# Kernel tuning notes

Measured on AMD Instinct MI355X. Metric: run time of the kernel, lower is better.

Reference implementation:

```python
import jax, jax.numpy as jnp
import numpy as np

B, S, H, NH = 2, 2048, 1024, 16
HD = H // NH  # head_dim = 64
ROPE_BASE = 10000.0


def _rope(x):
    # x: [B, NH, S, HD]; LLaMA-style half-split rotary embedding
    s, d = x.shape[2], x.shape[3]
    inv_freq = 1.0 / (ROPE_BASE ** (jnp.arange(0, d, 2, dtype=jnp.float32) / d))  # [d/2]
    ang = jnp.arange(s, dtype=jnp.float32)[:, None] * inv_freq[None, :]            # [S, d/2]
    cos, sin = jnp.cos(ang), jnp.sin(ang)
    x1, x2 = x[..., : d // 2], x[..., d // 2:]
    return jnp.concatenate([x1 * cos - x2 * sin, x1 * sin + x2 * cos], axis=-1)


def setup_inputs() -> dict:
    key = jax.random.key(0)
    ks = jax.random.split(key, 9)
    hidden_states = jax.random.normal(ks[0], (B, S, H), dtype=jnp.float32)
    # causal mask: True = attend
    causal = jnp.tril(jnp.ones((S, S), dtype=bool))
    attention_mask = jnp.broadcast_to(causal[None, None, :, :], (B, 1, S, S))
    std = 0.02
    wq = jax.random.normal(ks[1], (H, NH * HD), dtype=jnp.float32) * std
    wk = jax.random.normal(ks[2], (H, NH * HD), dtype=jnp.float32) * std
    wv = jax.random.normal(ks[3], (H, NH * HD), dtype=jnp.float32) * std
    wo = jax.random.normal(ks[4], (NH * HD, H), dtype=jnp.float32) * std
    bq = jnp.zeros((NH * HD,), dtype=jnp.float32)
    bk = jnp.zeros((NH * HD,), dtype=jnp.float32)
    bv = jnp.zeros((NH * HD,), dtype=jnp.float32)
    bo = jnp.zeros((H,), dtype=jnp.float32)
    return {"hidden_states": hidden_states, "attention_mask": attention_mask,
            "wq": wq, "bq": bq, "wk": wk, "bk": bk, "wv": wv, "bv": bv,
            "wo": wo, "bo": bo}


def _split_heads(x):
    b, s, _ = x.shape
    return jnp.transpose(x.reshape(b, s, NH, HD), (0, 2, 1, 3))


def reference(hidden_states, attention_mask, wq, bq, wk, bk, wv, bv, wo, bo):
    q = _split_heads(hidden_states @ wq + bq)  # [B,NH,S,HD]
    k = _split_heads(hidden_states @ wk + bk)
    v = _split_heads(hidden_states @ wv + bv)
    q = _rope(q)
    k = _rope(k)
    scores = jnp.einsum('bhqd,bhkd->bhqk', q, k) / jnp.sqrt(jnp.float32(HD))
    scores = jnp.where(attention_mask, scores, jnp.float32(-1e9))
    weights = jax.nn.softmax(scores, axis=-1)
    attn = jnp.einsum('bhqk,bhkv->bhqv', weights, v)  # [B,NH,S,HD]
    attn = jnp.transpose(attn, (0, 2, 1, 3)).reshape(hidden_states.shape[0], attn.shape[2], H)
    return attn @ wo + bo
```

## Files before the change

### kernel.cpp

```cpp
#include <hip/hip_runtime.h>
#include <math.h>

typedef short bf16x8 __attribute__((ext_vector_type(8)));
typedef float f32x4  __attribute__((ext_vector_type(4)));

__device__ __forceinline__ unsigned short f2bf(float f) {
    union { float f; unsigned u; } v; v.f = f;
    unsigned r = v.u + 0x7FFFu + ((v.u >> 16) & 1u);
    return (unsigned short)(r >> 16);
}

#define GLDS16(gp, lp) __builtin_amdgcn_global_load_lds( \
    (const __attribute__((address_space(1))) void*)(gp), \
    (__attribute__((address_space(3))) void*)(lp), 16, 0, 0)


__global__ __launch_bounds__(256)
void prep(const float* __restrict__ X, unsigned short* __restrict__ Xb,
          const float* __restrict__ w0, const float* __restrict__ w1,
          const float* __restrict__ w2, const float* __restrict__ w3,
          unsigned short* o0, unsigned short* o1,
          unsigned short* o2, unsigned short* o3)
{
    const int z = blockIdx.z;
    if (z >= 4) {
        const int lb = (z - 4) * 256 + blockIdx.y * 16 + blockIdx.x;
        const size_t t = (size_t)lb * 256 + threadIdx.x;
        const float4 a = *(const float4*)(X + t * 8);
        const float4 b = *(const float4*)(X + t * 8 + 4);
        unsigned short u[8] = { f2bf(a.x), f2bf(a.y), f2bf(a.z), f2bf(a.w),
                                f2bf(b.x), f2bf(b.y), f2bf(b.z), f2bf(b.w) };
        *(int4*)(Xb + t * 8) = *(int4*)u;
        return;
    }
    const float* W; unsigned short* O;
    switch (z) {
        case 0: W = w0; O = o0; break;
        case 1: W = w1; O = o1; break;
        case 2: W = w2; O = o2; break;
        default: W = w3; O = o3; break;
    }
    __shared__ float T[64][65];
    const int tid = threadIdx.x;
    const int n0 = blockIdx.x * 64, k0 = blockIdx.y * 64;
    #pragma unroll
    for (int i = 0; i < 4; i++) {
        const int k = (tid >> 4) + i * 16, n4 = (tid & 15) * 4;
        const float4 v = *(const float4*)(W + (size_t)(k0 + k) * 1024 + n0 + n4);
        T[k][n4] = v.x; T[k][n4+1] = v.y; T[k][n4+2] = v.z; T[k][n4+3] = v.w;
    }
    __syncthreads();
    if (z == 3) {
        #pragma unroll
        for (int i = 0; i < 4; i++) {
            const int n = (tid >> 4) + i * 16, k4 = (tid & 15) * 4;
            unsigned short u[4];
            #pragma unroll
            for (int j = 0; j < 4; j++) {
                const int q = k4 + j;
                const int p = (q & 3) * 16 + (q >> 2);
                const int d = (p & 3) * 16 + (p >> 2);
                u[j] = f2bf(T[d][n]);
            }
            *(int2*)(O + (size_t)(n0 + n) * 1024 + k0 + k4) = *(int2*)u;
        }
    } else {
        #pragma unroll
        for (int i = 0; i < 4; i++) {
            const int n = (tid >> 4) + i * 16, k4 = (tid & 15) * 4;
            unsigned short u[4] = { f2bf(T[k4][n]), f2bf(T[k4+1][n]),
                                    f2bf(T[k4+2][n]), f2bf(T[k4+3][n]) };
            *(int2*)(O + (size_t)(n0 + n) * 1024 + k0 + k4) = *(int2*)u;
        }
    }
}

__global__ __launch_bounds__(256)
void qkv_gemm(const unsigned short* __restrict__ Xb,
              const unsigned short* __restrict__ Wtq, const unsigned short* __restrict__ Wtk,
              const unsigned short* __restrict__ Wtv,
              const float* __restrict__ bq, const float* __restrict__ bk,
              const float* __restrict__ bv,
              unsigned short* __restrict__ Qb, unsigned short* __restrict__ Kb,
              unsigned short* __restrict__ Vtb)
{
    const unsigned short* Wt; const float* bias; unsigned short* Out;
    const int z = blockIdx.z;
    if (z == 0)      { Wt = Wtq; bias = bq; Out = Qb; }
    else if (z == 1) { Wt = Wtk; bias = bk; Out = Kb; }
    else             { Wt = Wtv; bias = bv; Out = Vtb; }

    __shared__ unsigned short Sh[128 * 72];
    unsigned short* As = Sh;
    unsigned short* Bs = Sh + 128 * 32;
    unsigned short* T  = Sh;

    const int tid = threadIdx.x, lane = tid & 63, w = tid >> 6;
    const int quad = lane >> 4, c = lane & 15;
    const int wr = w >> 1, wc = w & 1;
    const int m0 = blockIdx.x * 128, n0 = blockIdx.y * 128;
    const int srow = lane >> 2, scol = (lane & 3) * 8;

    f32x4 acc[4][4];
    #pragma unroll
    for (int i = 0; i < 4; i++)
        #pragma unroll
        for (int j = 0; j < 4; j++) acc[i][j] = (f32x4){0.f, 0.f, 0.f, 0.f};

    for (int k0 = 0; k0 < 1024; k0 += 32) {
        #pragma unroll
        for (int j = 0; j < 2; j++) {
            const int r = w * 32 + j * 16;
            GLDS16(Xb + (size_t)(m0 + r + srow) * 1024 + k0 + scol, &As[r * 32]);
            GLDS16(Wt + (size_t)(n0 + r + srow) * 1024 + k0 + scol, &Bs[r * 32]);
        }
        __syncthreads();
        bf16x8 af[4], bf[4];
        #pragma unroll
        for (int rt = 0; rt < 4; rt++)
            af[rt] = *(const bf16x8*)&As[(wr * 64 + rt * 16 + c) * 32 + quad * 8];
        #pragma unroll
        for (int nt = 0; nt < 4; nt++)
            bf[nt] = *(const bf16x8*)&Bs[(wc * 64 + nt * 16 + c) * 32 + quad * 8];
        #pragma unroll
        for (int rt = 0; rt < 4; rt++)
            #pragma unroll
            for (int nt = 0; nt < 4; nt++)
                acc[rt][nt] = __builtin_amdgcn_mfma_f32_16x16x32_bf16(af[rt], bf[nt], acc[rt][nt], 0, 0, 0);
        __syncthreads();
    }

    float bv4[4];
    #pragma unroll
    for (int nt = 0; nt < 4; nt++) bv4[nt] = bias[n0 + wc * 64 + nt * 16 + c];

    if (z == 2) {
        const int b = m0 >> 11, sb = m0 & 2047;
        const int hgbase = n0 >> 6;
        #pragma unroll
        for (int h = 0; h < 2; h++) {
            if (wc == h) {
                #pragma unroll
                for (int rt = 0; rt < 4; rt++)
                    #pragma unroll
                    for (int reg = 0; reg < 4; reg++) {
                        const int s = wr * 64 + rt * 16 + quad * 4 + reg;
                        unsigned short u[4];
                        #pragma unroll
                        for (int nt = 0; nt < 4; nt++)
                            u[nt] = f2bf(acc[rt][nt][reg] + bv4[nt]);
                        *(int2*)&T[s * 72 + c * 4] = *(int2*)u;
                    }
            }
            __syncthreads();
            const int p = tid >> 2, s8 = (tid & 3) * 32;
            unsigned short* dstb = Vtb + ((size_t)(b * 16 + hgbase + h) * 64 + p) * 2048 + sb;
            #pragma unroll
            for (int jj = 0; jj < 32; jj += 8) {
                unsigned short u[8];
                #pragma unroll
                for (int j = 0; j < 8; j++) u[j] = T[(s8 + jj + j) * 72 + p];
                *(int4*)(dstb + s8 + jj) = *(int4*)u;
            }
            __syncthreads();
        }
        return;
    }

    const float kLn = 9.210340371976184f / 32.0f;
    const float TWO_PI_INV = 0.15915494309189535f;
    const float rv0 = expf(-(float)c * kLn) * TWO_PI_INV;
    const float rv1 = expf(-(float)(c + 16) * kLn) * TWO_PI_INV;
    const float qscale = (z == 0) ? 0.125f : 1.0f;

    #pragma unroll
    for (int rt = 0; rt < 4; rt++) {
        #pragma unroll
        for (int reg = 0; reg < 4; reg++) {
            const int m = m0 + wr * 64 + rt * 16 + quad * 4 + reg;
            const int b = m >> 11, s = m & 2047;
            float x0 = acc[rt][0][reg] + bv4[0];
            float x1 = acc[rt][1][reg] + bv4[1];
            float x2 = acc[rt][2][reg] + bv4[2];
            float x3 = acc[rt][3][reg] + bv4[3];
            float r0 = (float)s * rv0;  r0 -= floorf(r0);
            float r1 = (float)s * rv1;  r1 -= floorf(r1);
            const float sn0 = __builtin_amdgcn_sinf(r0);
            const float cs0 = __builtin_amdgcn_cosf(r0);
            const float sn1 = __builtin_amdgcn_sinf(r1);
            const float cs1 = __builtin_amdgcn_cosf(r1);
            const float y0 = (x0 * cs0 - x2 * sn0) * qscale;
            const float y2 = (x0 * sn0 + x2 * cs0) * qscale;
            const float y1 = (x1 * cs1 - x3 * sn1) * qscale;
            const float y3 = (x1 * sn1 + x3 * cs1) * qscale;
            const int h = (n0 + wc * 64) >> 6;
            unsigned short u[4] = { f2bf(y0), f2bf(y1), f2bf(y2), f2bf(y3) };
            unsigned short* dst = Out + ((size_t)(b * 16 + h) * 2048 + s) * 64;
            *(int2*)(dst + c * 4) = *(int2*)u;
        }
    }
}

__global__ __launch_bounds__(256)
void out_gemm(const unsigned short* __restrict__ Ab, const unsigned short* __restrict__ Wto,
              const float* __restrict__ bo, float* __restrict__ Out)
{
    __shared__ unsigned short As[64 * 32];
    __shared__ unsigned short Bs[128 * 32];
    const int tid = threadIdx.x, lane = tid & 63, w = tid >> 6;
    const int quad = lane >> 4, c = lane & 15;
    const int wr = w >> 1, wc = w & 1;
    const int m0 = blockIdx.x * 64, n0 = blockIdx.y * 128;
    const int srow = lane >> 2, scol = (lane & 3) * 8;

    f32x4 acc[2][4];
    #pragma unroll
    for (int i = 0; i < 2; i++)
        #pragma unroll
        for (int j = 0; j < 4; j++) acc[i][j] = (f32x4){0.f, 0.f, 0.f, 0.f};

    for (int k0 = 0; k0 < 1024; k0 += 32) {
        {
            const int r = w * 16;
            GLDS16(Ab + (size_t)(m0 + r + srow) * 1024 + k0 + scol, &As[r * 32]);
        }
        #pragma unroll
        for (int j = 0; j < 2; j++) {
            const int r = w * 32 + j * 16;
            GLDS16(Wto + (size_t)(n0 + r + srow) * 1024 + k0 + scol, &Bs[r * 32]);
        }
        __syncthreads();
        bf16x8 af[2], bf[4];
        #pragma unroll
        for (int rt = 0; rt < 2; rt++)
            af[rt] = *(const bf16x8*)&As[(wr * 32 + rt * 16 + c) * 32 + quad * 8];
        #pragma unroll
        for (int nt = 0; nt < 4; nt++)
            bf[nt] = *(const bf16x8*)&Bs[(wc * 64 + nt * 16 + c) * 32 + quad * 8];
        #pragma unroll
        for (int rt = 0; rt < 2; rt++)
            #pragma unroll
            for (int nt = 0; nt < 4; nt++)
                acc[rt][nt] = __builtin_amdgcn_mfma_f32_16x16x32_bf16(af[rt], bf[nt], acc[rt][nt], 0, 0, 0);
        __syncthreads();
    }
    #pragma unroll
    for (int rt = 0; rt < 2; rt++) {
        #pragma unroll
        for (int reg = 0; reg < 4; reg++) {
            const int m = m0 + wr * 32 + rt * 16 + quad * 4 + reg;
            #pragma unroll
            for (int nt = 0; nt < 4; nt++) {
                const int n = n0 + wc * 64 + nt * 16 + c;
                Out[(size_t)m * 1024 + n] = acc[rt][nt][reg] + bo[n];
            }
        }
    }
}

__global__ __launch_bounds__(512)
void attn_part(const unsigned short* __restrict__ Qb, const unsigned short* __restrict__ Kb,
               const unsigned short* __restrict__ Vtb, unsigned short* __restrict__ Ab,
               float* __restrict__ Opart, float* __restrict__ Lpart)
{
    __shared__ unsigned short Ks[64 * 72];
    __shared__ unsigned short Vs[65 * 72];
    __shared__ unsigned short Ps[8 * 16 * 72];

    const int tid = threadIdx.x, w = tid >> 6, lane = tid & 63;
    const int quad = lane >> 4, c = lane & 15;
    const int bh = blockIdx.y;
    const int x = blockIdx.x;
    int ip, start, len;
    if (x < 8)       { ip = 9 + x;  start = 0;  len = 16; }
    else if (x < 16) { ip = 24 - x; start = 16; len = 2 * ip - 16; }
    else             { ip = 24 - x; start = 0;  len = 2 * ip; }
    const int q0 = (ip - 1) * 128;
    const bool complete = (x >= 16);
    const size_t base = (size_t)bh * 2048 * 64;

    if (tid < 64) Vs[64 * 72 + tid] = 0x3F80;
    __syncthreads();
    const bf16x8 on0 = *(const bf16x8*)&Vs[64 * 72 + quad * 8];
    const bf16x8 on1 = *(const bf16x8*)&Vs[64 * 72 + 32 + quad * 8];

    const int qbase = q0 + w * 16;
    const int qrow  = qbase + c;
    const size_t qoff = base + (size_t)qrow * 64;
    const bf16x8 qf0 = *(const bf16x8*)(Qb + qoff + quad * 8);
    const bf16x8 qf1 = *(const bf16x8*)(Qb + qoff + 32 + quad * 8);

    f32x4 O[4], Osum;
    Osum = (f32x4){0.f, 0.f, 0.f, 0.f};
    #pragma unroll
    for (int nt = 0; nt < 4; nt++) O[nt] = (f32x4){0.f, 0.f, 0.f, 0.f};

    const int rs = tid >> 3, c8 = (tid & 7) * 8;

    int k0 = start * 64;
    int4 kreg = *(const int4*)(Kb  + base + (size_t)(k0 + rs) * 64 + c8);
    int4 vreg = *(const int4*)(Vtb + base + (size_t)rs * 2048 + k0 + c8);

    unsigned short* Pw = Ps + w * 16 * 72;

    for (int t = 0; t < len; t++, k0 += 64) {
        *(int4*)&Ks[(size_t)rs * 72 + c8] = kreg;
        *(int4*)&Vs[(size_t)rs * 72 + c8] = vreg;
        __syncthreads();

        if (t + 1 < len) {
            const int kn = k0 + 64;
            kreg = *(const int4*)(Kb  + base + (size_t)(kn + rs) * 64 + c8);
            vreg = *(const int4*)(Vtb + base + (size_t)rs * 2048 + kn + c8);
        }

        if (k0 <= qbase + 15) {
            const bool need_mask = (k0 + 63) > qbase;
            #pragma unroll
            for (int nt = 0; nt < 4; nt++) {
                const bf16x8 kf0 = *(const bf16x8*)&Ks[(nt * 16 + c) * 72 + quad * 8];
                const bf16x8 kf1 = *(const bf16x8*)&Ks[(nt * 16 + c) * 72 + 32 + quad * 8];
                f32x4 s4 = (f32x4){0.f, 0.f, 0.f, 0.f};
                s4 = __builtin_amdgcn_mfma_f32_16x16x32_bf16(kf0, qf0, s4, 0, 0, 0);
                s4 = __builtin_amdgcn_mfma_f32_16x16x32_bf16(kf1, qf1, s4, 0, 0, 0);
                const int keyb = k0 + nt * 16 + quad * 4;
                unsigned short u[4];
                #pragma unroll
                for (int reg = 0; reg < 4; reg++) {
                    float p = __expf(s4[reg]);
                    if (need_mask && (keyb + reg > qrow)) p = 0.f;
                    u[reg] = f2bf(p);
                }
                *(int2*)&Pw[c * 72 + nt * 16 + quad * 4] = *(int2*)u;
            }
            const bf16x8 pa0 = *(const bf16x8*)&Pw[c * 72 + quad * 8];
            const bf16x8 pa1 = *(const bf16x8*)&Pw[c * 72 + 32 + quad * 8];
            #pragma unroll
            for (int nt = 0; nt < 4; nt++) {
                const bf16x8 vb0 = *(const bf16x8*)&Vs[(nt * 16 + c) * 72 + quad * 8];
                const bf16x8 vb1 = *(const bf16x8*)&Vs[(nt * 16 + c) * 72 + 32 + quad * 8];
                O[nt] = __builtin_amdgcn_mfma_f32_16x16x32_bf16(pa0, vb0, O[nt], 0, 0, 0);
                O[nt] = __builtin_amdgcn_mfma_f32_16x16x32_bf16(pa1, vb1, O[nt], 0, 0, 0);
            }
            Osum = __builtin_amdgcn_mfma_f32_16x16x32_bf16(pa0, on0, Osum, 0, 0, 0);
            Osum = __builtin_amdgcn_mfma_f32_16x16x32_bf16(pa1, on1, Osum, 0, 0, 0);
        }
        __syncthreads();
    }

    if (complete) {
        const int b = bh >> 4, h = bh & 15;
        #pragma unroll
        for (int reg = 0; reg < 4; reg++) {
            const float inv = 1.0f / Osum[reg];
            const int q = qbase + quad * 4 + reg;
            unsigned short u[4];
            #pragma unroll
            for (int nt = 0; nt < 4; nt++) u[nt] = f2bf(O[nt][reg] * inv);
            unsigned short* dst = Ab + ((size_t)(b * 2048 + q)) * 1024 + h * 64;
            *(int2*)(dst + c * 4) = *(int2*)u;
        }
    } else {
        const int pslot = (ip - 9) * 2 + (start ? 1 : 0);
        float* Op = Opart + ((size_t)bh * 16 + pslot) * 8192;
        float* Lp = Lpart + (size_t)bh * 2048 + (size_t)pslot * 128;
        #pragma unroll
        for (int reg = 0; reg < 4; reg++) {
            const int row = w * 16 + quad * 4 + reg;
            float4 o4 = make_float4(O[0][reg], O[1][reg], O[2][reg], O[3][reg]);
            *(float4*)(Op + (size_t)row * 64 + c * 4) = o4;
            if (c == 0) Lp[row] = Osum[reg];
        }
    }
}

__global__ __launch_bounds__(256)
void attn_combine(const float* __restrict__ Opart, const float* __restrict__ Lpart,
                  unsigned short* __restrict__ Ab)
{
    const int tid = threadIdx.x;
    const int j = blockIdx.x, bh = blockIdx.y;
    const int q0 = (8 + j) * 128;
    const size_t s0 = ((size_t)bh * 16 + j * 2) * 8192;
    const size_t l0 = (size_t)bh * 2048 + (size_t)j * 2 * 128;

    __shared__ float linv[128];
    if (tid < 128) linv[tid] = 1.0f / (Lpart[l0 + tid] + Lpart[l0 + 128 + tid]);
    __syncthreads();

    const int row = tid >> 1, col0 = (tid & 1) * 32;
    const float inv = linv[row];
    const int b = bh >> 4, h = bh & 15;
    const int q = q0 + row;
    unsigned short* dst = Ab + ((size_t)(b * 2048 + q)) * 1024 + h * 64 + col0;
    #pragma unroll
    for (int c4 = 0; c4 < 32; c4 += 4) {
        const float4 a  = *(const float4*)(Opart + s0 + (size_t)row * 64 + col0 + c4);
        const float4 bb = *(const float4*)(Opart + s0 + 8192 + (size_t)row * 64 + col0 + c4);
        dst[c4 + 0] = f2bf((a.x + bb.x) * inv);
        dst[c4 + 1] = f2bf((a.y + bb.y) * inv);
        dst[c4 + 2] = f2bf((a.z + bb.z) * inv);
        dst[c4 + 3] = f2bf((a.w + bb.w) * inv);
    }
}

extern "C" void kernel_launch(void* const* d_in, const int* in_sizes, int n_in,
                              void* d_out, int out_size, void* d_ws, size_t ws_size,
                              hipStream_t stream)
{
    const float* X  = (const float*)d_in[0];
    const float* wq = (const float*)d_in[2];
    const float* bq = (const float*)d_in[3];
    const float* wk = (const float*)d_in[4];
    const float* bk = (const float*)d_in[5];
    const float* wv = (const float*)d_in[6];
    const float* bv = (const float*)d_in[7];
    const float* wo = (const float*)d_in[8];
    const float* bo = (const float*)d_in[9];

    unsigned short* ws = (unsigned short*)d_ws;
    const size_t M1 = 1024 * 1024;
    unsigned short* Xb  = ws;
    unsigned short* Wtq = Xb  + 4 * M1;
    unsigned short* Wtk = Wtq + M1;
    unsigned short* Wtv = Wtk + M1;
    unsigned short* Wto = Wtv + M1;
    unsigned short* Qb  = Wto + M1;
    unsigned short* Kb  = Qb  + 4 * M1;
    unsigned short* Vtb = Kb  + 4 * M1;
    unsigned short* Ab  = Vtb + 4 * M1;
    float* Opart = (float*)(Ab + 4 * M1);
    float* Lpart = Opart + (size_t)32 * 16 * 8192;

    prep        <<<dim3(16, 16, 12), 256, 0, stream>>>(X, Xb, wq, wk, wv, wo,
                                                       Wtq, Wtk, Wtv, Wto);
    qkv_gemm    <<<dim3(32, 8, 3), 256, 0, stream>>>(Xb, Wtq, Wtk, Wtv, bq, bk, bv,
                                                     Qb, Kb, Vtb);
    attn_part   <<<dim3(24, 32), 512, 0, stream>>>(Qb, Kb, Vtb, Ab, Opart, Lpart);
    attn_combine<<<dim3(8, 32), 256, 0, stream>>>(Opart, Lpart, Ab);
    out_gemm    <<<dim3(64, 8), 256, 0, stream>>>(Ab, Wto, bo, (float*)d_out);
}
```

Baseline: 218.4 us.

## Process two 16-row query tiles per wave in attention with 256-thread blocks

The attention partial kernel now uses 4 waves of 256 threads, each handling 32 query rows as two 16-row tiles, so every K/V fragment read from LDS feeds twice as many MFMAs. Each thread loads two K and two V rows per step. Probabilities are packed to bf16 with the hardware v_cvt_pk_bf16_f32 instruction, and s_setprio brackets the MFMA sections. This raises register pressure and halves the waves per block, which may reduce latency hiding.

Result: slower. 226.7 us (+3.8%).

```diff
diff --git a/kernel.cpp b/kernel.cpp
--- a/kernel.cpp
+++ b/kernel.cpp
@@ -8,6 +8,12 @@
     union { float f; unsigned u; } v; v.f = f;
     unsigned r = v.u + 0x7FFFu + ((v.u >> 16) & 1u);
     return (unsigned short)(r >> 16);
+}
+
+__device__ __forceinline__ unsigned cvt_pk_bf16(float a, float b) {
+    unsigned r;
+    asm("v_cvt_pk_bf16_f32 %0, %1, %2" : "=v"(r) : "v"(a), "v"(b));
+    return r;
 }
 
 #define GLDS16(gp, lp) __builtin_amdgcn_global_load_lds( \
@@ -258,14 +264,14 @@
     }
 }
 
-__global__ __launch_bounds__(512)
+__global__ __launch_bounds__(256)
 void attn_part(const unsigned short* __restrict__ Qb, const unsigned short* __restrict__ Kb,
                const unsigned short* __restrict__ Vtb, unsigned short* __restrict__ Ab,
                float* __restrict__ Opart, float* __restrict__ Lpart)
 {
     __shared__ unsigned short Ks[64 * 72];
-    __shared__ unsigned short Vs[65 * 72];
-    __shared__ unsigned short Ps[8 * 16 * 72];
+    __shared__ unsigned short Vs[64 * 72];
+    __shared__ unsigned short Ps[4 * 32 * 72];
 
     const int tid = threadIdx.x, w = tid >> 6, lane = tid & 63;
     const int quad = lane >> 4, c = lane & 15;
@@ -279,71 +285,118 @@
     const bool complete = (x >= 16);
     const size_t base = (size_t)bh * 2048 * 64;
 
-    if (tid < 64) Vs[64 * 72 + tid] = 0x3F80;
-    __syncthreads();
-    const bf16x8 on0 = *(const bf16x8*)&Vs[64 * 72 + quad * 8];
-    const bf16x8 on1 = *(const bf16x8*)&Vs[64 * 72 + 32 + quad * 8];
-
-    const int qbase = q0 + w * 16;
-    const int qrow  = qbase + c;
-    const size_t qoff = base + (size_t)qrow * 64;
-    const bf16x8 qf0 = *(const bf16x8*)(Qb + qoff + quad * 8);
-    const bf16x8 qf1 = *(const bf16x8*)(Qb + qoff + 32 + quad * 8);
-
-    f32x4 O[4], Osum;
-    Osum = (f32x4){0.f, 0.f, 0.f, 0.f};
-    #pragma unroll
-    for (int nt = 0; nt < 4; nt++) O[nt] = (f32x4){0.f, 0.f, 0.f, 0.f};
+    bf16x8 on;
+    #pragma unroll
+    for (int i = 0; i < 8; i++) on[i] = (short)0x3F80;
+
+    const int qbase = q0 + w * 32;
+    const size_t qoffA = base + (size_t)(qbase + c) * 64;
+    const size_t qoffB = base + (size_t)(qbase + 16 + c) * 64;
+    const bf16x8 qfA0 = *(const bf16x8*)(Qb + qoffA + quad * 8);
+    const bf16x8 qfA1 = *(const bf16x8*)(Qb + qoffA + 32 + quad * 8);
+    const bf16x8 qfB0 = *(const bf16x8*)(Qb + qoffB + quad * 8);
+    const bf16x8 qfB1 = *(const bf16x8*)(Qb + qoffB + 32 + quad * 8);
+
+    f32x4 OA[4], OB[4], OsA, OsB;
+    OsA = (f32x4){0.f, 0.f, 0.f, 0.f};
+    OsB = (f32x4){0.f, 0.f, 0.f, 0.f};
+    #pragma unroll
+    for (int nt = 0; nt < 4; nt++) { OA[nt] = OsA; OB[nt] = OsA; }
 
     const int rs = tid >> 3, c8 = (tid & 7) * 8;
 
     int k0 = start * 64;
-    int4 kreg = *(const int4*)(Kb  + base + (size_t)(k0 + rs) * 64 + c8);
-    int4 vreg = *(const int4*)(Vtb + base + (size_t)rs * 2048 + k0 + c8);
-
-    unsigned short* Pw = Ps + w * 16 * 72;
+    int4 kr0 = *(const int4*)(Kb  + base + (size_t)(k0 + rs) * 64 + c8);
+    int4 kr1 = *(const int4*)(Kb  + base + (size_t)(k0 + rs + 32) * 64 + c8);
+    int4 vr0 = *(const int4*)(Vtb + base + (size_t)rs * 2048 + k0 + c8);
+    int4 vr1 = *(const int4*)(Vtb + base + (size_t)(rs + 32) * 2048 + k0 + c8);
+
+    unsigned short* Pw = Ps + w * 32 * 72;
 
     for (int t = 0; t < len; t++, k0 += 64) {
-        *(int4*)&Ks[(size_t)rs * 72 + c8] = kreg;
-        *(int4*)&Vs[(size_t)rs * 72 + c8] = vreg;
+        *(int4*)&Ks[(size_t)rs * 72 + c8] = kr0;
+        *(int4*)&Ks[(size_t)(rs + 32) * 72 + c8] = kr1;
+        *(int4*)&Vs[(size_t)rs * 72 + c8] = vr0;
+        *(int4*)&Vs[(size_t)(rs + 32) * 72 + c8] = vr1;
         __syncthreads();
 
         if (t + 1 < len) {
             const int kn = k0 + 64;
-            kreg = *(const int4*)(Kb  + base + (size_t)(kn + rs) * 64 + c8);
-            vreg = *(const int4*)(Vtb + base + (size_t)rs * 2048 + kn + c8);
-        }
-
-        if (k0 <= qbase + 15) {
-            const bool need_mask = (k0 + 63) > qbase;
+            kr0 = *(const int4*)(Kb  + base + (size_t)(kn + rs) * 64 + c8);
+            kr1 = *(const int4*)(Kb  + base + (size_t)(kn + rs + 32) * 64 + c8);
+            vr0 = *(const int4*)(Vtb + base + (size_t)rs * 2048 + kn + c8);
+            vr1 = *(const int4*)(Vtb + base + (size_t)(rs + 32) * 2048 + kn + c8);
+        }
+
+        if (k0 <= qbase + 31) {
+            f32x4 sA[4], sB[4];
+            __builtin_amdgcn_s_setprio(1);
             #pragma unroll
             for (int nt = 0; nt < 4; nt++) {
                 const bf16x8 kf0 = *(const bf16x8*)&Ks[(nt * 16 + c) * 72 + quad * 8];
                 const bf16x8 kf1 = *(const bf16x8*)&Ks[(nt * 16 + c) * 72 + 32 + quad * 8];
-                f32x4 s4 = (f32x4){0.f, 0.f, 0.f, 0.f};
-                s4 = __builtin_amdgcn_mfma_f32_16x16x32_bf16(kf0, qf0, s4, 0, 0, 0);
-                s4 = __builtin_amdgcn_mfma_f32_16x16x32_bf16(kf1, qf1, s4, 0, 0, 0);
-                const int keyb = k0 + nt * 16 + quad * 4;
-                unsigned short u[4];
+                const f32x4 z = (f32x4){0.f, 0.f, 0.f, 0.f};
+                sA[nt] = __builtin_amdgcn_mfma_f32_16x16x32_bf16(kf0, qfA0, z, 0, 0, 0);
+                sA[nt] = __builtin_amdgcn_mfma_f32_16x16x32_bf16(kf1, qfA1, sA[nt], 0, 0, 0);
+                sB[nt] = __builtin_amdgcn_mfma_f32_16x16x32_bf16(kf0, qfB0, z, 0, 0, 0);
+                sB[nt] = __builtin_amdgcn_mfma_f32_16x16x32_bf16(kf1, qfB1, sB[nt], 0, 0, 0);
+            }
+            __builtin_amdgcn_s_setprio(0);
+
+            {
+                const int qrow = qbase + c;
+                const bool nm = (k0 + 63) > qbase;
                 #pragma unroll
-                for (int reg = 0; reg < 4; reg++) {
-                    float p = __expf(s4[reg]);
-                    if (need_mask && (keyb + reg > qrow)) p = 0.f;
-                    u[reg] = f2bf(p);
+                for (int nt = 0; nt < 4; nt++) {
+                    const int keyb = k0 + nt * 16 + quad * 4;
+                    float p[4];
+                    #pragma unroll
+                    for (int r = 0; r < 4; r++) {
+                        float pv = __expf(sA[nt][r]);
+                        if (nm && (keyb + r > qrow)) pv = 0.f;
+                        p[r] = pv;
+                    }
+                    unsigned u[2] = { cvt_pk_bf16(p[0], p[1]), cvt_pk_bf16(p[2], p[3]) };
+                    *(int2*)&Pw[c * 72 + nt * 16 + quad * 4] = *(int2*)u;
                 }
-                *(int2*)&Pw[c * 72 + nt * 16 + quad * 4] = *(int2*)u;
-            }
-            const bf16x8 pa0 = *(const bf16x8*)&Pw[c * 72 + quad * 8];
-            const bf16x8 pa1 = *(const bf16x8*)&Pw[c * 72 + 32 + quad * 8];
+            }
+            {
+                const int qrow = qbase + 16 + c;
+                const bool nm = (k0 + 63) > (qbase + 16);
+                #pragma unroll
+                for (int nt = 0; nt < 4; nt++) {
+                    const int keyb = k0 + nt * 16 + quad * 4;
+                    float p[4];
+                    #pragma unroll
+                    for (int r = 0; r < 4; r++) {
+                        float pv = __expf(sB[nt][r]);
+                        if (nm && (keyb + r > qrow)) pv = 0.f;
+                        p[r] = pv;
+                    }
+                    unsigned u[2] = { cvt_pk_bf16(p[0], p[1]), cvt_pk_bf16(p[2], p[3]) };
+                    *(int2*)&Pw[(16 + c) * 72 + nt * 16 + quad * 4] = *(int2*)u;
+                }
+            }
+
+            const bf16x8 paA0 = *(const bf16x8*)&Pw[c * 72 + quad * 8];
+            const bf16x8 paA1 = *(const bf16x8*)&Pw[c * 72 + 32 + quad * 8];
+            const bf16x8 paB0 = *(const bf16x8*)&Pw[(16 + c) * 72 + quad * 8];
+            const bf16x8 paB1 = *(const bf16x8*)&Pw[(16 + c) * 72 + 32 + quad * 8];
+            __builtin_amdgcn_s_setprio(1);
             #pragma unroll
             for (int nt = 0; nt < 4; nt++) {
                 const bf16x8 vb0 = *(const bf16x8*)&Vs[(nt * 16 + c) * 72 + quad * 8];
                 const bf16x8 vb1 = *(const bf16x8*)&Vs[(nt * 16 + c) * 72 + 32 + quad * 8];
-                O[nt] = __builtin_amdgcn_mfma_f32_16x16x32_bf16(pa0, vb0, O[nt], 0, 0, 0);
-                O[nt] = __builtin_amdgcn_mfma_f32_16x16x32_bf16(pa1, vb1, O[nt], 0, 0, 0);
-            }
-            Osum = __builtin_amdgcn_mfma_f32_16x16x32_bf16(pa0, on0, Osum, 0, 0, 0);
-            Osum = __builtin_amdgcn_mfma_f32_16x16x32_bf16(pa1, on1, Osum, 0, 0, 0);
+                OA[nt] = __builtin_amdgcn_mfma_f32_16x16x32_bf16(paA0, vb0, OA[nt], 0, 0, 0);
+                OA[nt] = __builtin_amdgcn_mfma_f32_16x16x32_bf16(paA1, vb1, OA[nt], 0, 0, 0);
+                OB[nt] = __builtin_amdgcn_mfma_f32_16x16x32_bf16(paB0, vb0, OB[nt], 0, 0, 0);
+                OB[nt] = __builtin_amdgcn_mfma_f32_16x16x32_bf16(paB1, vb1, OB[nt], 0, 0, 0);
+            }
+            OsA = __builtin_amdgcn_mfma_f32_16x16x32_bf16(paA0, on, OsA, 0, 0, 0);
+            OsA = __builtin_amdgcn_mfma_f32_16x16x32_bf16(paA1, on, OsA, 0, 0, 0);
+            OsB = __builtin_amdgcn_mfma_f32_16x16x32_bf16(paB0, on, OsB, 0, 0, 0);
+            OsB = __builtin_amdgcn_mfma_f32_16x16x32_bf16(paB1, on, OsB, 0, 0, 0);
+            __builtin_amdgcn_s_setprio(0);
         }
         __syncthreads();
     }
@@ -352,13 +405,21 @@
         const int b = bh >> 4, h = bh & 15;
         #pragma unroll
         for (int reg = 0; reg < 4; reg++) {
-            const float inv = 1.0f / Osum[reg];
-            const int q = qbase + quad * 4 + reg;
-            unsigned short u[4];
-            #pragma unroll
-            for (int nt = 0; nt < 4; nt++) u[nt] = f2bf(O[nt][reg] * inv);
-            unsigned short* dst = Ab + ((size_t)(b * 2048 + q)) * 1024 + h * 64;
-            *(int2*)(dst + c * 4) = *(int2*)u;
+            const float invA = 1.0f / OsA[reg];
+            const int qA = qbase + quad * 4 + reg;
+            unsigned short uA[4];
+            #pragma unroll
+            for (int nt = 0; nt < 4; nt++) uA[nt] = f2bf(OA[nt][reg] * invA);
+            unsigned short* dA = Ab + ((size_t)(b * 2048 + qA)) * 1024 + h * 64;
+            *(int2*)(dA + c * 4) = *(int2*)uA;
+
+            const float invB = 1.0f / OsB[reg];
+            const int qB = qbase + 16 + quad * 4 + reg;
+            unsigned short uB[4];
+            #pragma unroll
+            for (int nt = 0; nt < 4; nt++) uB[nt] = f2bf(OB[nt][reg] * invB);
+            unsigned short* dB = Ab + ((size_t)(b * 2048 + qB)) * 1024 + h * 64;
+            *(int2*)(dB + c * 4) = *(int2*)uB;
         }
     } else {
         const int pslot = (ip - 9) * 2 + (start ? 1 : 0);
@@ -366,10 +427,15 @@
         float* Lp = Lpart + (size_t)bh * 2048 + (size_t)pslot * 128;
         #pragma unroll
         for (int reg = 0; reg < 4; reg++) {
-            const int row = w * 16 + quad * 4 + reg;
-            float4 o4 = make_float4(O[0][reg], O[1][reg], O[2][reg], O[3][reg]);
-            *(float4*)(Op + (size_t)row * 64 + c * 4) = o4;
-            if (c == 0) Lp[row] = Osum[reg];
+            const int rowA = w * 32 + quad * 4 + reg;
+            float4 oA = make_float4(OA[0][reg], OA[1][reg], OA[2][reg], OA[3][reg]);
+            *(float4*)(Op + (size_t)rowA * 64 + c * 4) = oA;
+            if (c == 0) Lp[rowA] = OsA[reg];
+
+            const int rowB = rowA + 16;
+            float4 oB = make_float4(OB[0][reg], OB[1][reg], OB[2][reg], OB[3][reg]);
+            *(float4*)(Op + (size_t)rowB * 64 + c * 4) = oB;
+            if (c == 0) Lp[rowB] = OsB[reg];
         }
     }
 }
@@ -436,7 +502,7 @@
                                                        Wtq, Wtk, Wtv, Wto);
     qkv_gemm    <<<dim3(32, 8, 3), 256, 0, stream>>>(Xb, Wtq, Wtk, Wtv, bq, bk, bv,
                                                      Qb, Kb, Vtb);
-    attn_part   <<<dim3(24, 32), 512, 0, stream>>>(Qb, Kb, Vtb, Ab, Opart, Lpart);
+    attn_part   <<<dim3(24, 32), 256, 0, stream>>>(Qb, Kb, Vtb, Ab, Opart, Lpart);
     attn_combine<<<dim3(8, 32), 256, 0, stream>>>(Opart, Lpart, Ab);
     out_gemm    <<<dim3(64, 8), 256, 0, stream>>>(Ab, Wto, bo, (float*)d_out);
 }
```

## Keep attention probabilities in registers instead of round-tripping through LDS

Applied to the files above, without the earlier changes.

The exp'd scores from the QK MFMA are packed straight into the A operand of the PV MFMA using v_cvt_pk_bf16_f32. The V fragment reads are permuted to match that register layout of the key dimension, which removes the per-wave P buffer in shared memory along with its store and reload. The ones vector is now built in registers instead of shared memory, and s_setprio brackets the compute section. This cuts LDS traffic and LDS footprint, and may raise occupancy. The risk is that the permuted V reads must exactly match the MFMA k-index ordering, and the 8-byte LDS reads are narrower.

Result: faster. 211.4 us (-3.2%).

```diff
diff --git a/kernel.cpp b/kernel.cpp
--- a/kernel.cpp
+++ b/kernel.cpp
@@ -2,12 +2,19 @@
 #include <math.h>
 
 typedef short bf16x8 __attribute__((ext_vector_type(8)));
+typedef short bf16x4 __attribute__((ext_vector_type(4)));
 typedef float f32x4  __attribute__((ext_vector_type(4)));
 
 __device__ __forceinline__ unsigned short f2bf(float f) {
     union { float f; unsigned u; } v; v.f = f;
     unsigned r = v.u + 0x7FFFu + ((v.u >> 16) & 1u);
     return (unsigned short)(r >> 16);
+}
+
+__device__ __forceinline__ unsigned cvt_pk_bf16(float a, float b) {
+    unsigned r;
+    asm("v_cvt_pk_bf16_f32 %0, %1, %2" : "=v"(r) : "v"(a), "v"(b));
+    return r;
 }
 
 #define GLDS16(gp, lp) __builtin_amdgcn_global_load_lds( \
@@ -264,8 +271,7 @@
                float* __restrict__ Opart, float* __restrict__ Lpart)
 {
     __shared__ unsigned short Ks[64 * 72];
-    __shared__ unsigned short Vs[65 * 72];
-    __shared__ unsigned short Ps[8 * 16 * 72];
+    __shared__ unsigned short Vs[64 * 72];
 
     const int tid = threadIdx.x, w = tid >> 6, lane = tid & 63;
     const int quad = lane >> 4, c = lane & 15;
@@ -279,10 +285,9 @@
     const bool complete = (x >= 16);
     const size_t base = (size_t)bh * 2048 * 64;
 
-    if (tid < 64) Vs[64 * 72 + tid] = 0x3F80;
-    __syncthreads();
-    const bf16x8 on0 = *(const bf16x8*)&Vs[64 * 72 + quad * 8];
-    const bf16x8 on1 = *(const bf16x8*)&Vs[64 * 72 + 32 + quad * 8];
+    bf16x8 on;
+    #pragma unroll
+    for (int i = 0; i < 8; i++) on[i] = (short)0x3F80;
 
     const int qbase = q0 + w * 16;
     const int qrow  = qbase + c;
@@ -301,7 +306,8 @@
     int4 kreg = *(const int4*)(Kb  + base + (size_t)(k0 + rs) * 64 + c8);
     int4 vreg = *(const int4*)(Vtb + base + (size_t)rs * 2048 + k0 + c8);
 
-    unsigned short* Pw = Ps + w * 16 * 72;
+    union P8 { bf16x8 v8; unsigned wd[4]; };
+    union V8 { bf16x8 v8; bf16x4 v4[2]; };
 
     for (int t = 0; t < len; t++, k0 += 64) {
         *(int4*)&Ks[(size_t)rs * 72 + c8] = kreg;
@@ -316,6 +322,8 @@
 
         if (k0 <= qbase + 15) {
             const bool need_mask = (k0 + 63) > qbase;
+            P8 pa0, pa1;
+            __builtin_amdgcn_s_setprio(1);
             #pragma unroll
             for (int nt = 0; nt < 4; nt++) {
                 const bf16x8 kf0 = *(const bf16x8*)&Ks[(nt * 16 + c) * 72 + quad * 8];
@@ -324,26 +332,33 @@
                 s4 = __builtin_amdgcn_mfma_f32_16x16x32_bf16(kf0, qf0, s4, 0, 0, 0);
                 s4 = __builtin_amdgcn_mfma_f32_16x16x32_bf16(kf1, qf1, s4, 0, 0, 0);
                 const int keyb = k0 + nt * 16 + quad * 4;
-                unsigned short u[4];
+                float p[4];
                 #pragma unroll
                 for (int reg = 0; reg < 4; reg++) {
-                    float p = __expf(s4[reg]);
-                    if (need_mask && (keyb + reg > qrow)) p = 0.f;
-                    u[reg] = f2bf(p);
+                    float pv = __expf(s4[reg]);
+                    if (need_mask && (keyb + reg > qrow)) pv = 0.f;
+                    p[reg] = pv;
                 }
-                *(int2*)&Pw[c * 72 + nt * 16 + quad * 4] = *(int2*)u;
-            }
-            const bf16x8 pa0 = *(const bf16x8*)&Pw[c * 72 + quad * 8];
-            const bf16x8 pa1 = *(const bf16x8*)&Pw[c * 72 + 32 + quad * 8];
+                const unsigned wa = cvt_pk_bf16(p[0], p[1]);
+                const unsigned wb = cvt_pk_bf16(p[2], p[3]);
+                if (nt < 2) { pa0.wd[2 * nt]     = wa; pa0.wd[2 * nt + 1]     = wb; }
+                else        { pa1.wd[2 * (nt-2)] = wa; pa1.wd[2 * (nt-2) + 1] = wb; }
+            }
+
             #pragma unroll
             for (int nt = 0; nt < 4; nt++) {
-                const bf16x8 vb0 = *(const bf16x8*)&Vs[(nt * 16 + c) * 72 + quad * 8];
-                const bf16x8 vb1 = *(const bf16x8*)&Vs[(nt * 16 + c) * 72 + 32 + quad * 8];
-                O[nt] = __builtin_amdgcn_mfma_f32_16x16x32_bf16(pa0, vb0, O[nt], 0, 0, 0);
-                O[nt] = __builtin_amdgcn_mfma_f32_16x16x32_bf16(pa1, vb1, O[nt], 0, 0, 0);
-            }
-            Osum = __builtin_amdgcn_mfma_f32_16x16x32_bf16(pa0, on0, Osum, 0, 0, 0);
-            Osum = __builtin_amdgcn_mfma_f32_16x16x32_bf16(pa1, on1, Osum, 0, 0, 0);
+                const int pr = (nt * 16 + c) * 72 + 4 * quad;
+                V8 vb0, vb1;
+                vb0.v4[0] = *(const bf16x4*)&Vs[pr];
+                vb0.v4[1] = *(const bf16x4*)&Vs[pr + 16];
+                vb1.v4[0] = *(const bf16x4*)&Vs[pr + 32];
+                vb1.v4[1] = *(const bf16x4*)&Vs[pr + 48];
+                O[nt] = __builtin_amdgcn_mfma_f32_16x16x32_bf16(pa0.v8, vb0.v8, O[nt], 0, 0, 0);
+                O[nt] = __builtin_amdgcn_mfma_f32_16x16x32_bf16(pa1.v8, vb1.v8, O[nt], 0, 0, 0);
+            }
+            Osum = __builtin_amdgcn_mfma_f32_16x16x32_bf16(pa0.v8, on, Osum, 0, 0, 0);
+            Osum = __builtin_amdgcn_mfma_f32_16x16x32_bf16(pa1.v8, on, Osum, 0, 0, 0);
+            __builtin_amdgcn_s_setprio(0);
         }
         __syncthreads();
     }
```
